# Optimization experiments

Hardware: AMD Instinct MI355X
Metric: run time of the kernel (lower is better)

## Reference

```python
import jax, jax.numpy as jnp
import numpy as np

N, C, H, W = 8, 192, 64, 64
CQK = 24  # C // ratio with ratio=8


def setup_inputs() -> dict:
    key = jax.random.key(0)
    k1, k2, k3, k4 = jax.random.split(key, 4)
    x = jax.random.normal(k1, (N, C, H, W), dtype=jnp.float32)
    Wq = jax.random.normal(k2, (CQK, C), dtype=jnp.float32) * (1.0 / np.sqrt(C))
    Wk = jax.random.normal(k3, (CQK, C), dtype=jnp.float32) * (1.0 / np.sqrt(C))
    Wv = jax.random.normal(k4, (C, C), dtype=jnp.float32) * (1.0 / np.sqrt(C))
    return {"x": x, "Wq": Wq, "Wk": Wk, "Wv": Wv}


def reference(x, Wq, Wk, Wv):
    n, c, h, w = x.shape
    xf = x.reshape(n, c, h * w)                       # [n, C, L]
    q = jnp.einsum('oc,ncl->nol', Wq, xf)             # [n, CQK, L] (1x1 conv)
    k = jnp.einsum('oc,ncl->nol', Wk, xf)             # [n, CQK, L]
    v = jnp.einsum('oc,ncl->nol', Wv, xf)             # [n, C, L]
    # mask[n, l, m] = softmax_m( q[:, :, l] . k[:, :, m] )  -- no scaling in original
    scores = jnp.einsum('nol,nom->nlm', q, k)         # [n, L, L]
    mask = jax.nn.softmax(scores, axis=-1)
    # feat = v @ mask^T : feat[n, c, l] = sum_m v[n, c, m] * mask[n, l, m]
    feat = jnp.einsum('ncm,nlm->ncl', v, mask)
    return feat.reshape(n, c, h, w)
```

## Files before the change

kernel.cpp:

```cpp
#include <hip/hip_runtime.h>
#include <hip/hip_bf16.h>

#define L 4096
#define NB 8
#define C 192
#define CQK 24
#define DP 32
#define QBLK 64
#define KBLK 64
#define NT (L / KBLK)
#define BN 64
#define XS_W 200
#define LOG2E 1.4426950408889634f

typedef _Float16 half_t;
typedef __fp16 fp16x2 __attribute__((ext_vector_type(2)));
typedef __fp16 fp16x4 __attribute__((ext_vector_type(4)));
typedef _Float16 half8 __attribute__((ext_vector_type(8)));
typedef float f32x4 __attribute__((ext_vector_type(4)));


__global__ __launch_bounds__(256, 2) void proj_mfma(const float* __restrict__ x,
                                                    const float* __restrict__ Wq,
                                                    const float* __restrict__ Wk,
                                                    const float* __restrict__ Wv,
                                                    half_t* __restrict__ Qh,
                                                    half_t* __restrict__ Kh,
                                                    half_t* __restrict__ Vh) {
  __shared__ half_t Xs[BN][XS_W];
  __shared__ half_t Qt[BN][DP];
  __shared__ half_t Kt[BN][DP];

  int tid = threadIdx.x;
  int lane = tid & 63;
  int wave = tid >> 6;
  int li = lane & 15;
  int g = lane >> 4;

  int blk = blockIdx.x;
  int n = blk >> 6;
  int l0 = (blk & 63) * BN;

  const float* xbase = x + (size_t)n * C * L + l0;
#pragma unroll
  for (int it = 0; it < 12; ++it) {
    int fid = it * 256 + tid;
    int l4 = fid & 15;
    int c = fid >> 4;
    f32x4 v = *reinterpret_cast<const f32x4*>(xbase + (size_t)c * L + l4 * 4);
#pragma unroll
    for (int j = 0; j < 4; ++j) Xs[l4 * 4 + j][c] = (half_t)v[j];
  }
  __syncthreads();

  const float* rowp[4];
  bool rvalid[4];
#pragma unroll
  for (int mt = 0; mt < 4; ++mt) {
    int row = wave * 64 + mt * 16 + li;
    const float* p;
    bool v = true;
    if (row < 32) {
      v = row < CQK;
      p = Wq + (size_t)(v ? row : 0) * C;
    } else if (row < 64) {
      v = (row - 32) < CQK;
      p = Wk + (size_t)(v ? row - 32 : 0) * C;
    } else {
      p = Wv + (size_t)(row - 64) * C;
    }
    rowp[mt] = p;
    rvalid[mt] = v;
  }

  f32x4 acc[4][4];
#pragma unroll
  for (int mt = 0; mt < 4; ++mt)
#pragma unroll
    for (int nt = 0; nt < 4; ++nt) acc[mt][nt] = {0.f, 0.f, 0.f, 0.f};

  half8 az;
#pragma unroll
  for (int j = 0; j < 8; ++j) az[j] = (half_t)0.f;

#pragma unroll
  for (int kk = 0; kk < 6; ++kk) {
    half8 af[4];
#pragma unroll
    for (int mt = 0; mt < 4; ++mt) {
      const float* p = rowp[mt] + kk * 32 + g * 8;
      f32x4 w0 = *reinterpret_cast<const f32x4*>(p);
      f32x4 w1 = *reinterpret_cast<const f32x4*>(p + 4);
      half8 a;
#pragma unroll
      for (int j = 0; j < 4; ++j) {
        a[j] = (half_t)w0[j];
        a[4 + j] = (half_t)w1[j];
      }
      af[mt] = rvalid[mt] ? a : az;
    }
#pragma unroll
    for (int nt = 0; nt < 4; ++nt) {
      half8 b = *reinterpret_cast<const half8*>(&Xs[nt * 16 + li][kk * 32 + g * 8]);
#pragma unroll
      for (int mt = 0; mt < 4; ++mt)
        acc[mt][nt] = __builtin_amdgcn_mfma_f32_16x16x32_f16(af[mt], b, acc[mt][nt], 0, 0, 0);
    }
  }

  if (wave >= 1) {
#pragma unroll
    for (int mt = 0; mt < 4; ++mt)
#pragma unroll
      for (int nt = 0; nt < 4; ++nt)
#pragma unroll
        for (int r = 0; r < 4; ++r) {
          int c = (wave - 1) * 64 + mt * 16 + 4 * g + r;
          int l = nt * 16 + li;
          Vh[((size_t)n * C + c) * L + l0 + l] = (half_t)acc[mt][nt][r];
        }
  } else {
#pragma unroll
    for (int mt = 0; mt < 4; ++mt)
#pragma unroll
      for (int nt = 0; nt < 4; ++nt)
#pragma unroll
        for (int r = 0; r < 4; ++r) {
          int o = (mt & 1) * 16 + 4 * g + r;
          int l = nt * 16 + li;
          if (mt < 2) Qt[l][o] = (half_t)(acc[mt][nt][r] * LOG2E);
          else        Kt[l][o] = (half_t)acc[mt][nt][r];
        }
  }
  __syncthreads();

  if (tid < 128) {
    int which = tid >> 6;
    int l = tid & 63;
    const half8* src = reinterpret_cast<const half8*>(which ? &Kt[l][0] : &Qt[l][0]);
    half_t* dstp = (which ? Kh : Qh) + ((size_t)n * L + l0 + l) * DP;
    half8* dst = reinterpret_cast<half8*>(dstp);
#pragma unroll
    for (int i = 0; i < 4; ++i) dst[i] = src[i];
  }
}


struct SMemA {
  half_t P[2][QBLK][64];
  float rs[2][QBLK];
  float Ls[QBLK];
};

__global__ __launch_bounds__(256, 2) void attn(const half_t* __restrict__ Qh,
                                               const half_t* __restrict__ Kh,
                                               const half_t* __restrict__ Vh,
                                               float* __restrict__ out) {
  __shared__ SMemA sm;

  const int tid = threadIdx.x;
  const int wave = tid >> 6;
  const int lane = tid & 63;
  const int li = lane & 15;
  const int g = lane >> 4;
  const int n = blockIdx.x;
  const int q0 = blockIdx.y * QBLK;
  const int c0 = wave * 48;
  const int swz = (li & 7) << 4;

  const half8 qfrag = *reinterpret_cast<const half8*>(
      Qh + ((size_t)(n * L + q0 + wave * 16 + li)) * DP + g * 8);

  const char* kb = (const char*)(Kh + (size_t)n * L * DP) +
                   ((size_t)li * DP + g * 8) * 2;
  const char* vb[3];
  vb[0] = (const char*)(Vh + (size_t)n * C * L) +
          ((size_t)(c0 + li) * L + g * 8) * 2;
  vb[1] = vb[0] + (size_t)16 * L * 2;
  vb[2] = vb[0] + (size_t)32 * L * 2;

  f32x4 acc[3][4];
#pragma unroll
  for (int ct = 0; ct < 3; ++ct)
#pragma unroll
    for (int qt = 0; qt < 4; ++qt) acc[ct][qt] = {0.f, 0.f, 0.f, 0.f};

  float Lrow = 0.f;
  float coff = -28.f;

  half8 kA[4], vA[6], kB[4], vB[6];

#pragma unroll
  for (int b = 0; b < 4; ++b)
    kA[b] = *reinterpret_cast<const half8*>(kb + b * 1024);
  kb += KBLK * DP * 2;
#pragma unroll
  for (int ct = 0; ct < 3; ++ct) {
    vA[ct * 2 + 0] = *reinterpret_cast<const half8*>(vb[ct]);
    vA[ct * 2 + 1] = *reinterpret_cast<const half8*>(vb[ct] + 64);
    vb[ct] += KBLK * 2;
  }

  auto phase = [&](const half8(&kc)[4], const half8(&vc)[6], half8(&kn)[4],
                   half8(&vn)[6], int t) {
    const int par = t & 1;
    if (t + 1 < NT) {
#pragma unroll
      for (int b = 0; b < 4; ++b)
        kn[b] = *reinterpret_cast<const half8*>(kb + b * 1024);
      kb += KBLK * DP * 2;
#pragma unroll
      for (int ct = 0; ct < 3; ++ct) {
        vn[ct * 2 + 0] = *reinterpret_cast<const half8*>(vb[ct]);
        vn[ct * 2 + 1] = *reinterpret_cast<const half8*>(vb[ct] + 64);
        vb[ct] += KBLK * 2;
      }
    }

    f32x4 cvec = {coff, coff, coff, coff};
    f32x4 s[4];
#pragma unroll
    for (int b = 0; b < 4; ++b)
      s[b] = __builtin_amdgcn_mfma_f32_16x16x32_f16(kc[b], qfrag, cvec, 0, 0, 0);

    float p[4][4];
    float mx = -1.0e30f;
#pragma unroll
    for (int b = 0; b < 4; ++b) {
      mx = fmaxf(mx, fmaxf(fmaxf(s[b][0], s[b][1]), fmaxf(s[b][2], s[b][3])));
#pragma unroll
      for (int r = 0; r < 4; ++r) p[b][r] = __builtin_amdgcn_exp2f(s[b][r]);
    }

    float sc = 1.0f;
    if (__any((int)(mx > 15.f))) {
      float m2 = fmaxf(mx, __shfl_xor(mx, 16));
      m2 = fmaxf(m2, __shfl_xor(m2, 32));
      if (m2 > 15.f) {
        sc = __builtin_amdgcn_exp2f(-m2);
        Lrow *= sc;
        coff -= m2;
#pragma unroll
        for (int b = 0; b < 4; ++b)
#pragma unroll
          for (int r = 0; r < 4; ++r)
            p[b][r] = __builtin_amdgcn_exp2f(s[b][r] - m2);
      }
    }

#pragma unroll
    for (int b = 0; b < 4; ++b)
#pragma unroll
      for (int r = 0; r < 4; ++r) Lrow += p[b][r];

    {
      char* prow = (char*)&sm.P[par][wave * 16 + li][0];
#pragma unroll
      for (int b = 0; b < 4; ++b) {
        fp16x2 lo = __builtin_amdgcn_cvt_pkrtz(p[b][0], p[b][1]);
        fp16x2 hi = __builtin_amdgcn_cvt_pkrtz(p[b][2], p[b][3]);
        fp16x4 h = __builtin_shufflevector(lo, hi, 0, 1, 2, 3);
        *reinterpret_cast<fp16x4*>(prow + ((b * 32 + 8 * g) ^ swz)) = h;
      }
    }
    if (lane < 16) sm.rs[par][wave * 16 + li] = sc;

    asm volatile("s_waitcnt lgkmcnt(0)\n\ts_barrier" ::: "memory");

    {
      f32x4 f = {sm.rs[par][li], sm.rs[par][16 + li], sm.rs[par][32 + li],
                 sm.rs[par][48 + li]};
      bool an = (f[0] != 1.f) || (f[1] != 1.f) || (f[2] != 1.f) || (f[3] != 1.f);
      if (__any((int)an)) {
#pragma unroll
        for (int ct = 0; ct < 3; ++ct)
#pragma unroll
          for (int qt = 0; qt < 4; ++qt) acc[ct][qt] *= f[qt];
      }
    }

#pragma unroll
    for (int ch = 0; ch < 2; ++ch)
#pragma unroll
      for (int qt = 0; qt < 4; ++qt) {
        const char* prow = (const char*)&sm.P[par][qt * 16 + li][0];
        half8 pfrag = *reinterpret_cast<const half8*>(
            prow + ((ch * 64 + 16 * g) ^ swz));
#pragma unroll
        for (int ct = 0; ct < 3; ++ct)
          acc[ct][qt] = __builtin_amdgcn_mfma_f32_16x16x32_f16(
              vc[ct * 2 + ch], pfrag, acc[ct][qt], 0, 0, 0);
      }
  };

  for (int t = 0; t < NT; t += 2) {
    phase(kA, vA, kB, vB, t);
    phase(kB, vB, kA, vA, t + 1);
  }

  float sum = Lrow;
  sum += __shfl_xor(sum, 16);
  sum += __shfl_xor(sum, 32);
  if (lane < 16) sm.Ls[wave * 16 + li] = sum;
  __syncthreads();

  float inv[4];
#pragma unroll
  for (int qt = 0; qt < 4; ++qt) inv[qt] = 1.0f / sm.Ls[qt * 16 + li];

#pragma unroll
  for (int ct = 0; ct < 3; ++ct)
#pragma unroll
    for (int qt = 0; qt < 4; ++qt)
#pragma unroll
      for (int r = 0; r < 4; ++r)
        out[((size_t)n * C + c0 + ct * 16 + 4 * g + r) * L + q0 + qt * 16 + li] =
            acc[ct][qt][r] * inv[qt];
}


extern "C" void kernel_launch(void* const* d_in, const int* in_sizes, int n_in,
                              void* d_out, int out_size, void* d_ws, size_t ws_size,
                              hipStream_t stream) {
  (void)in_sizes; (void)n_in; (void)out_size; (void)ws_size;
  const float* x = (const float*)d_in[0];
  const float* Wq = (const float*)d_in[1];
  const float* Wk = (const float*)d_in[2];
  const float* Wv = (const float*)d_in[3];
  float* out = (float*)d_out;

  half_t* Qh = (half_t*)d_ws;
  half_t* Kh = Qh + (size_t)NB * L * DP;
  half_t* Vh = Kh + (size_t)NB * L * DP;

  hipLaunchKernelGGL(proj_mfma, dim3(NB * (L / BN)), dim3(256), 0, stream,
                     x, Wq, Wk, Wv, Qh, Kh, Vh);
  hipLaunchKernelGGL(attn, dim3(NB, L / QBLK), dim3(256), 0, stream,
                     Qh, Kh, Vh, out);
}
```

Measured before the change: 146.2 us.

## Software-pipeline QK softmax one tile ahead of PV with single barrier per tile

Restructures the attention loop so each iteration computes scores and writes P for tile t+1 while running the PV MFMAs for tile t from the other shared-memory buffer, leaving one barrier per tile instead of a strict QK→barrier→PV sequence. K is prefetched two tiles ahead and V one tile ahead. The rescale factors and row sums are re-laid out as [li*4+wave] so each lane reads them as one vector load. The aim is to overlap exp/softmax ALU work and LDS writes with PV matrix work; it adds prologue/epilogue code and raises register pressure.

Result: faster. 142.8 us (-2.3%).

```diff
diff --git a/kernel.cpp b/kernel.cpp
--- a/kernel.cpp
+++ b/kernel.cpp
@@ -171,8 +171,8 @@
   const half8 qfrag = *reinterpret_cast<const half8*>(
       Qh + ((size_t)(n * L + q0 + wave * 16 + li)) * DP + g * 8);
 
-  const char* kb = (const char*)(Kh + (size_t)n * L * DP) +
-                   ((size_t)li * DP + g * 8) * 2;
+  const char* kptr = (const char*)(Kh + (size_t)n * L * DP) +
+                     ((size_t)li * DP + g * 8) * 2;
   const char* vb[3];
   vb[0] = (const char*)(Vh + (size_t)n * C * L) +
           ((size_t)(c0 + li) * L + g * 8) * 2;
@@ -190,39 +190,7 @@
 
   half8 kA[4], vA[6], kB[4], vB[6];
 
-#pragma unroll
-  for (int b = 0; b < 4; ++b)
-    kA[b] = *reinterpret_cast<const half8*>(kb + b * 1024);
-  kb += KBLK * DP * 2;
-#pragma unroll
-  for (int ct = 0; ct < 3; ++ct) {
-    vA[ct * 2 + 0] = *reinterpret_cast<const half8*>(vb[ct]);
-    vA[ct * 2 + 1] = *reinterpret_cast<const half8*>(vb[ct] + 64);
-    vb[ct] += KBLK * 2;
-  }
-
-  auto phase = [&](const half8(&kc)[4], const half8(&vc)[6], half8(&kn)[4],
-                   half8(&vn)[6], int t) {
-    const int par = t & 1;
-    if (t + 1 < NT) {
-#pragma unroll
-      for (int b = 0; b < 4; ++b)
-        kn[b] = *reinterpret_cast<const half8*>(kb + b * 1024);
-      kb += KBLK * DP * 2;
-#pragma unroll
-      for (int ct = 0; ct < 3; ++ct) {
-        vn[ct * 2 + 0] = *reinterpret_cast<const half8*>(vb[ct]);
-        vn[ct * 2 + 1] = *reinterpret_cast<const half8*>(vb[ct] + 64);
-        vb[ct] += KBLK * 2;
-      }
-    }
-
-    f32x4 cvec = {coff, coff, coff, coff};
-    f32x4 s[4];
-#pragma unroll
-    for (int b = 0; b < 4; ++b)
-      s[b] = __builtin_amdgcn_mfma_f32_16x16x32_f16(kc[b], qfrag, cvec, 0, 0, 0);
-
+  auto sm_write = [&](const f32x4(&s)[4], int par) {
     float p[4][4];
     float mx = -1.0e30f;
 #pragma unroll
@@ -231,7 +199,6 @@
 #pragma unroll
       for (int r = 0; r < 4; ++r) p[b][r] = __builtin_amdgcn_exp2f(s[b][r]);
     }
-
     float sc = 1.0f;
     if (__any((int)(mx > 15.f))) {
       float m2 = fmaxf(mx, __shfl_xor(mx, 16));
@@ -247,38 +214,34 @@
             p[b][r] = __builtin_amdgcn_exp2f(s[b][r] - m2);
       }
     }
-
 #pragma unroll
     for (int b = 0; b < 4; ++b)
 #pragma unroll
       for (int r = 0; r < 4; ++r) Lrow += p[b][r];
 
-    {
-      char* prow = (char*)&sm.P[par][wave * 16 + li][0];
-#pragma unroll
-      for (int b = 0; b < 4; ++b) {
-        fp16x2 lo = __builtin_amdgcn_cvt_pkrtz(p[b][0], p[b][1]);
-        fp16x2 hi = __builtin_amdgcn_cvt_pkrtz(p[b][2], p[b][3]);
-        fp16x4 h = __builtin_shufflevector(lo, hi, 0, 1, 2, 3);
-        *reinterpret_cast<fp16x4*>(prow + ((b * 32 + 8 * g) ^ swz)) = h;
-      }
-    }
-    if (lane < 16) sm.rs[par][wave * 16 + li] = sc;
-
-    asm volatile("s_waitcnt lgkmcnt(0)\n\ts_barrier" ::: "memory");
-
-    {
-      f32x4 f = {sm.rs[par][li], sm.rs[par][16 + li], sm.rs[par][32 + li],
-                 sm.rs[par][48 + li]};
-      bool an = (f[0] != 1.f) || (f[1] != 1.f) || (f[2] != 1.f) || (f[3] != 1.f);
-      if (__any((int)an)) {
-#pragma unroll
-        for (int ct = 0; ct < 3; ++ct)
-#pragma unroll
-          for (int qt = 0; qt < 4; ++qt) acc[ct][qt] *= f[qt];
-      }
-    }
-
+    char* prow = (char*)&sm.P[par][wave * 16 + li][0];
+#pragma unroll
+    for (int b = 0; b < 4; ++b) {
+      fp16x2 lo = __builtin_amdgcn_cvt_pkrtz(p[b][0], p[b][1]);
+      fp16x2 hi = __builtin_amdgcn_cvt_pkrtz(p[b][2], p[b][3]);
+      fp16x4 h = __builtin_shufflevector(lo, hi, 0, 1, 2, 3);
+      *reinterpret_cast<fp16x4*>(prow + ((b * 32 + 8 * g) ^ swz)) = h;
+    }
+    if (lane < 16) sm.rs[par][li * 4 + wave] = sc;
+  };
+
+  auto apply_rescale = [&](int par) {
+    f32x4 f = *reinterpret_cast<const f32x4*>(&sm.rs[par][li * 4]);
+    bool an = (f[0] != 1.f) | (f[1] != 1.f) | (f[2] != 1.f) | (f[3] != 1.f);
+    if (__any((int)an)) {
+#pragma unroll
+      for (int ct = 0; ct < 3; ++ct)
+#pragma unroll
+        for (int qt = 0; qt < 4; ++qt) acc[ct][qt] *= f[qt];
+    }
+  };
+
+  auto pv = [&](const half8(&vp)[6], int par) {
 #pragma unroll
     for (int ch = 0; ch < 2; ++ch)
 #pragma unroll
@@ -289,24 +252,81 @@
 #pragma unroll
         for (int ct = 0; ct < 3; ++ct)
           acc[ct][qt] = __builtin_amdgcn_mfma_f32_16x16x32_f16(
-              vc[ct * 2 + ch], pfrag, acc[ct][qt], 0, 0, 0);
+              vp[ct * 2 + ch], pfrag, acc[ct][qt], 0, 0, 0);
       }
   };
 
-  for (int t = 0; t < NT; t += 2) {
-    phase(kA, vA, kB, vB, t);
-    phase(kB, vB, kA, vA, t + 1);
-  }
+#pragma unroll
+  for (int b = 0; b < 4; ++b)
+    kA[b] = *reinterpret_cast<const half8*>(kptr + b * 1024);
+  kptr += KBLK * DP * 2;
+#pragma unroll
+  for (int b = 0; b < 4; ++b)
+    kB[b] = *reinterpret_cast<const half8*>(kptr + b * 1024);
+  kptr += KBLK * DP * 2;
+#pragma unroll
+  for (int ct = 0; ct < 3; ++ct) {
+    vA[ct * 2 + 0] = *reinterpret_cast<const half8*>(vb[ct]);
+    vA[ct * 2 + 1] = *reinterpret_cast<const half8*>(vb[ct] + 64);
+    vb[ct] += KBLK * 2;
+  }
+  {
+    f32x4 cvec = {coff, coff, coff, coff};
+    f32x4 s[4];
+#pragma unroll
+    for (int b = 0; b < 4; ++b)
+      s[b] = __builtin_amdgcn_mfma_f32_16x16x32_f16(kA[b], qfrag, cvec, 0, 0, 0);
+    sm_write(s, 0);
+  }
+  asm volatile("s_waitcnt lgkmcnt(0)\n\ts_barrier" ::: "memory");
+
+  auto phase = [&](const half8(&kq)[4], const half8(&vp)[6], half8(&kd)[4],
+                   half8(&vd)[6], int par, bool doK) {
+    if (doK) {
+#pragma unroll
+      for (int b = 0; b < 4; ++b)
+        kd[b] = *reinterpret_cast<const half8*>(kptr + b * 1024);
+      kptr += KBLK * DP * 2;
+    }
+#pragma unroll
+    for (int ct = 0; ct < 3; ++ct) {
+      vd[ct * 2 + 0] = *reinterpret_cast<const half8*>(vb[ct]);
+      vd[ct * 2 + 1] = *reinterpret_cast<const half8*>(vb[ct] + 64);
+      vb[ct] += KBLK * 2;
+    }
+
+    f32x4 cvec = {coff, coff, coff, coff};
+    f32x4 s[4];
+#pragma unroll
+    for (int b = 0; b < 4; ++b)
+      s[b] = __builtin_amdgcn_mfma_f32_16x16x32_f16(kq[b], qfrag, cvec, 0, 0, 0);
+
+    apply_rescale(par);
+    pv(vp, par);
+
+    sm_write(s, par ^ 1);
+    asm volatile("s_waitcnt lgkmcnt(0)\n\ts_barrier" ::: "memory");
+  };
+
+  for (int t = 0; t < 62; t += 2) {
+    phase(kB, vA, kA, vB, 0, true);
+    phase(kA, vB, kB, vA, 1, true);
+  }
+  phase(kB, vA, kA, vB, 0, false);
+
+  apply_rescale(1);
+  pv(vB, 1);
 
   float sum = Lrow;
   sum += __shfl_xor(sum, 16);
   sum += __shfl_xor(sum, 32);
-  if (lane < 16) sm.Ls[wave * 16 + li] = sum;
+  if (lane < 16) sm.Ls[li * 4 + wave] = sum;
   __syncthreads();
 
+  f32x4 Lv = *reinterpret_cast<const f32x4*>(&sm.Ls[li * 4]);
   float inv[4];
 #pragma unroll
-  for (int qt = 0; qt < 4; ++qt) inv[qt] = 1.0f / sm.Ls[qt * 16 + li];
+  for (int qt = 0; qt < 4; ++qt) inv[qt] = 1.0f / Lv[qt];
 
 #pragma unroll
   for (int ct = 0; ct < 3; ++ct)
```

## Rewrite attention kernel with 32x32 MFMA and register-only P exchange

Applied to the files above, without the earlier changes.

Replaces the 16x16x32 MFMA attention loop with 32x32x16 MFMAs. Each wave now owns 32 queries and 96 channels, so the probability tile stays in registers and is rearranged into the B-operand layout with cross-half lane shuffles. This drops the shared-memory P buffer, the per-tile block barrier and the shared rescale factors. In exchange, each wave recomputes scores for its query pair (duplicating QK work across the two channel-half waves), loses the double-buffered K/V prefetch for V, and uses more registers per wave.

Result: slower. 227.6 us (+55.7%).

```diff
diff --git a/kernel.cpp b/kernel.cpp
--- a/kernel.cpp
+++ b/kernel.cpp
@@ -18,6 +18,7 @@
 typedef __fp16 fp16x4 __attribute__((ext_vector_type(4)));
 typedef _Float16 half8 __attribute__((ext_vector_type(8)));
 typedef float f32x4 __attribute__((ext_vector_type(4)));
+typedef float f32x16 __attribute__((ext_vector_type(16)));
 
 
 __global__ __launch_bounds__(256, 2) void proj_mfma(const float* __restrict__ x,
@@ -146,176 +147,141 @@
 }
 
 
-struct SMemA {
-  half_t P[2][QBLK][64];
-  float rs[2][QBLK];
-  float Ls[QBLK];
-};
-
 __global__ __launch_bounds__(256, 2) void attn(const half_t* __restrict__ Qh,
                                                const half_t* __restrict__ Kh,
                                                const half_t* __restrict__ Vh,
                                                float* __restrict__ out) {
-  __shared__ SMemA sm;
-
   const int tid = threadIdx.x;
   const int wave = tid >> 6;
   const int lane = tid & 63;
-  const int li = lane & 15;
-  const int g = lane >> 4;
+  const int qp = lane & 31;
+  const int h = lane >> 5;
+  const int qg = wave >> 1;
+  const int ch = wave & 1;
   const int n = blockIdx.x;
-  const int q0 = blockIdx.y * QBLK;
-  const int c0 = wave * 48;
-  const int swz = (li & 7) << 4;
-
-  const half8 qfrag = *reinterpret_cast<const half8*>(
-      Qh + ((size_t)(n * L + q0 + wave * 16 + li)) * DP + g * 8);
-
-  const char* kb = (const char*)(Kh + (size_t)n * L * DP) +
-                   ((size_t)li * DP + g * 8) * 2;
-  const char* vb[3];
-  vb[0] = (const char*)(Vh + (size_t)n * C * L) +
-          ((size_t)(c0 + li) * L + g * 8) * 2;
-  vb[1] = vb[0] + (size_t)16 * L * 2;
-  vb[2] = vb[0] + (size_t)32 * L * 2;
-
-  f32x4 acc[3][4];
-#pragma unroll
-  for (int ct = 0; ct < 3; ++ct)
-#pragma unroll
-    for (int qt = 0; qt < 4; ++qt) acc[ct][qt] = {0.f, 0.f, 0.f, 0.f};
+  const int q0 = blockIdx.y * QBLK + qg * 32;
+  const int c0w = ch * 96;
+
+  const half_t* qb = Qh + ((size_t)(n * L + q0 + qp)) * DP + h * 8;
+  const half8 qf0 = *reinterpret_cast<const half8*>(qb);
+  const half8 qf1 = *reinterpret_cast<const half8*>(qb + 16);
+
+  const half_t* kp = Kh + (size_t)n * L * DP + (size_t)qp * DP + h * 8;
+  const half_t* vp = Vh + (size_t)n * C * L + (size_t)(c0w + qp) * L + h * 8;
+
+  f32x16 acc[3];
+#pragma unroll
+  for (int cb = 0; cb < 3; ++cb)
+#pragma unroll
+    for (int r = 0; r < 16; ++r) acc[cb][r] = 0.f;
 
   float Lrow = 0.f;
   float coff = -28.f;
 
-  half8 kA[4], vA[6], kB[4], vB[6];
-
-#pragma unroll
-  for (int b = 0; b < 4; ++b)
-    kA[b] = *reinterpret_cast<const half8*>(kb + b * 1024);
-  kb += KBLK * DP * 2;
-#pragma unroll
-  for (int ct = 0; ct < 3; ++ct) {
-    vA[ct * 2 + 0] = *reinterpret_cast<const half8*>(vb[ct]);
-    vA[ct * 2 + 1] = *reinterpret_cast<const half8*>(vb[ct] + 64);
-    vb[ct] += KBLK * 2;
-  }
-
-  auto phase = [&](const half8(&kc)[4], const half8(&vc)[6], half8(&kn)[4],
-                   half8(&vn)[6], int t) {
-    const int par = t & 1;
+  half8 kf[2][2];
+  half8 vf[3][4];
+
+#pragma unroll
+  for (int mb = 0; mb < 2; ++mb)
+#pragma unroll
+    for (int c2 = 0; c2 < 2; ++c2)
+      kf[mb][c2] = *reinterpret_cast<const half8*>(kp + mb * 32 * DP + c2 * 16);
+  kp += (size_t)KBLK * DP;
+
+  for (int t = 0; t < NT; ++t) {
+#pragma unroll
+    for (int cb = 0; cb < 3; ++cb)
+#pragma unroll
+      for (int ck = 0; ck < 4; ++ck)
+        vf[cb][ck] = *reinterpret_cast<const half8*>(vp + (size_t)cb * 32 * L + ck * 16);
+    vp += KBLK;
+
+    f32x16 cvec;
+#pragma unroll
+    for (int r = 0; r < 16; ++r) cvec[r] = coff;
+    f32x16 s0 = __builtin_amdgcn_mfma_f32_32x32x16_f16(kf[0][0], qf0, cvec, 0, 0, 0);
+    s0 = __builtin_amdgcn_mfma_f32_32x32x16_f16(kf[0][1], qf1, s0, 0, 0, 0);
+    f32x16 s1 = __builtin_amdgcn_mfma_f32_32x32x16_f16(kf[1][0], qf0, cvec, 0, 0, 0);
+    s1 = __builtin_amdgcn_mfma_f32_32x32x16_f16(kf[1][1], qf1, s1, 0, 0, 0);
+
     if (t + 1 < NT) {
 #pragma unroll
-      for (int b = 0; b < 4; ++b)
-        kn[b] = *reinterpret_cast<const half8*>(kb + b * 1024);
-      kb += KBLK * DP * 2;
-#pragma unroll
-      for (int ct = 0; ct < 3; ++ct) {
-        vn[ct * 2 + 0] = *reinterpret_cast<const half8*>(vb[ct]);
-        vn[ct * 2 + 1] = *reinterpret_cast<const half8*>(vb[ct] + 64);
-        vb[ct] += KBLK * 2;
+      for (int mb = 0; mb < 2; ++mb)
+#pragma unroll
+        for (int c2 = 0; c2 < 2; ++c2)
+          kf[mb][c2] = *reinterpret_cast<const half8*>(kp + mb * 32 * DP + c2 * 16);
+      kp += (size_t)KBLK * DP;
+    }
+
+    float mx = -1.0e30f;
+#pragma unroll
+    for (int r = 0; r < 16; ++r) mx = fmaxf(mx, fmaxf(s0[r], s1[r]));
+    float rm = fmaxf(mx, __shfl_xor(mx, 32));
+    if (__any((int)(rm > 15.f))) {
+      float adj = rm > 15.f ? rm : 0.f;
+      float sc = __builtin_amdgcn_exp2f(-adj);
+      Lrow *= sc;
+      coff -= adj;
+#pragma unroll
+      for (int r = 0; r < 16; ++r) { s0[r] -= adj; s1[r] -= adj; }
+#pragma unroll
+      for (int cb = 0; cb < 3; ++cb)
+#pragma unroll
+        for (int r = 0; r < 16; ++r) acc[cb][r] *= sc;
+    }
+#pragma unroll
+    for (int r = 0; r < 16; ++r) {
+      s0[r] = __builtin_amdgcn_exp2f(s0[r]);
+      s1[r] = __builtin_amdgcn_exp2f(s1[r]);
+      Lrow += s0[r] + s1[r];
+    }
+
+    int u_[2][4][2];
+#pragma unroll
+    for (int s2 = 0; s2 < 4; ++s2)
+#pragma unroll
+      for (int i = 0; i < 2; ++i) {
+        union { fp16x2 v; int w; } a, b;
+        a.v = __builtin_amdgcn_cvt_pkrtz(s0[4 * s2 + 2 * i], s0[4 * s2 + 2 * i + 1]);
+        b.v = __builtin_amdgcn_cvt_pkrtz(s1[4 * s2 + 2 * i], s1[4 * s2 + 2 * i + 1]);
+        u_[0][s2][i] = a.w;
+        u_[1][s2][i] = b.w;
       }
-    }
-
-    f32x4 cvec = {coff, coff, coff, coff};
-    f32x4 s[4];
-#pragma unroll
-    for (int b = 0; b < 4; ++b)
-      s[b] = __builtin_amdgcn_mfma_f32_16x16x32_f16(kc[b], qfrag, cvec, 0, 0, 0);
-
-    float p[4][4];
-    float mx = -1.0e30f;
-#pragma unroll
-    for (int b = 0; b < 4; ++b) {
-      mx = fmaxf(mx, fmaxf(fmaxf(s[b][0], s[b][1]), fmaxf(s[b][2], s[b][3])));
-#pragma unroll
-      for (int r = 0; r < 4; ++r) p[b][r] = __builtin_amdgcn_exp2f(s[b][r]);
-    }
-
-    float sc = 1.0f;
-    if (__any((int)(mx > 15.f))) {
-      float m2 = fmaxf(mx, __shfl_xor(mx, 16));
-      m2 = fmaxf(m2, __shfl_xor(m2, 32));
-      if (m2 > 15.f) {
-        sc = __builtin_amdgcn_exp2f(-m2);
-        Lrow *= sc;
-        coff -= m2;
-#pragma unroll
-        for (int b = 0; b < 4; ++b)
-#pragma unroll
-          for (int r = 0; r < 4; ++r)
-            p[b][r] = __builtin_amdgcn_exp2f(s[b][r] - m2);
-      }
-    }
-
-#pragma unroll
-    for (int b = 0; b < 4; ++b)
-#pragma unroll
-      for (int r = 0; r < 4; ++r) Lrow += p[b][r];
-
-    {
-      char* prow = (char*)&sm.P[par][wave * 16 + li][0];
-#pragma unroll
-      for (int b = 0; b < 4; ++b) {
-        fp16x2 lo = __builtin_amdgcn_cvt_pkrtz(p[b][0], p[b][1]);
-        fp16x2 hi = __builtin_amdgcn_cvt_pkrtz(p[b][2], p[b][3]);
-        fp16x4 h = __builtin_shufflevector(lo, hi, 0, 1, 2, 3);
-        *reinterpret_cast<fp16x4*>(prow + ((b * 32 + 8 * g) ^ swz)) = h;
-      }
-    }
-    if (lane < 16) sm.rs[par][wave * 16 + li] = sc;
-
-    asm volatile("s_waitcnt lgkmcnt(0)\n\ts_barrier" ::: "memory");
-
-    {
-      f32x4 f = {sm.rs[par][li], sm.rs[par][16 + li], sm.rs[par][32 + li],
-                 sm.rs[par][48 + li]};
-      bool an = (f[0] != 1.f) || (f[1] != 1.f) || (f[2] != 1.f) || (f[3] != 1.f);
-      if (__any((int)an)) {
-#pragma unroll
-        for (int ct = 0; ct < 3; ++ct)
-#pragma unroll
-          for (int qt = 0; qt < 4; ++qt) acc[ct][qt] *= f[qt];
-      }
-    }
-
-#pragma unroll
-    for (int ch = 0; ch < 2; ++ch)
-#pragma unroll
-      for (int qt = 0; qt < 4; ++qt) {
-        const char* prow = (const char*)&sm.P[par][qt * 16 + li][0];
-        half8 pfrag = *reinterpret_cast<const half8*>(
-            prow + ((ch * 64 + 16 * g) ^ swz));
-#pragma unroll
-        for (int ct = 0; ct < 3; ++ct)
-          acc[ct][qt] = __builtin_amdgcn_mfma_f32_16x16x32_f16(
-              vc[ct * 2 + ch], pfrag, acc[ct][qt], 0, 0, 0);
-      }
-  };
-
-  for (int t = 0; t < NT; t += 2) {
-    phase(kA, vA, kB, vB, t);
-    phase(kB, vB, kA, vA, t + 1);
-  }
-
-  float sum = Lrow;
-  sum += __shfl_xor(sum, 16);
-  sum += __shfl_xor(sum, 32);
-  if (lane < 16) sm.Ls[wave * 16 + li] = sum;
-  __syncthreads();
-
-  float inv[4];
-#pragma unroll
-  for (int qt = 0; qt < 4; ++qt) inv[qt] = 1.0f / sm.Ls[qt * 16 + li];
-
-#pragma unroll
-  for (int ct = 0; ct < 3; ++ct)
-#pragma unroll
-    for (int qt = 0; qt < 4; ++qt)
-#pragma unroll
-      for (int r = 0; r < 4; ++r)
-        out[((size_t)n * C + c0 + ct * 16 + 4 * g + r) * L + q0 + qt * 16 + li] =
-            acc[ct][qt][r] * inv[qt];
+
+    int x_[2][2][2];
+#pragma unroll
+    for (int mb = 0; mb < 2; ++mb)
+#pragma unroll
+      for (int c1 = 0; c1 < 2; ++c1)
+#pragma unroll
+        for (int i = 0; i < 2; ++i)
+          x_[mb][c1][i] =
+              __shfl_xor(h ? u_[mb][2 * c1][i] : u_[mb][2 * c1 + 1][i], 32);
+
+#pragma unroll
+    for (int ck = 0; ck < 4; ++ck) {
+      const int mb = ck >> 1, c1 = ck & 1;
+      union { int w[4]; half8 v; } pb;
+      pb.w[0] = h ? x_[mb][c1][0] : u_[mb][2 * c1][0];
+      pb.w[1] = h ? x_[mb][c1][1] : u_[mb][2 * c1][1];
+      pb.w[2] = h ? u_[mb][2 * c1 + 1][0] : x_[mb][c1][0];
+      pb.w[3] = h ? u_[mb][2 * c1 + 1][1] : x_[mb][c1][1];
+#pragma unroll
+      for (int cb = 0; cb < 3; ++cb)
+        acc[cb] = __builtin_amdgcn_mfma_f32_32x32x16_f16(vf[cb][ck], pb.v, acc[cb], 0, 0, 0);
+    }
+  }
+
+  float sum = Lrow + __shfl_xor(Lrow, 32);
+  float inv = 1.0f / sum;
+
+#pragma unroll
+  for (int cb = 0; cb < 3; ++cb)
+#pragma unroll
+    for (int r = 0; r < 16; ++r) {
+      int c = c0w + cb * 32 + (r & 3) + 8 * (r >> 2) + 4 * h;
+      out[((size_t)n * C + c) * L + q0 + qp] = acc[cb][r] * inv;
+    }
 }
 
 
```
